# Optimization experiments

Measured on AMD Instinct MI355X. Metric: run time of the kernel, lower is better.

## Reference

```python
import jax, jax.numpy as jnp
import numpy as np

N = 16384          # total points
B = 2              # scans; points[:,0] is batch id
K = 16             # knn neighbors (includes self, dist 0)
CH = [4, 16, 16, 32, 32]
EPS = 1e-5


def setup_inputs() -> dict:
    key = jax.random.key(0)
    ks = jax.random.split(key, 1 + len(CH) - 1)
    feat = jax.random.normal(ks[0], (N, 4), dtype=jnp.float32)
    bidx = jnp.repeat(jnp.arange(B, dtype=jnp.float32), N // B)
    points = jnp.concatenate([bidx[:, None], feat], axis=1)  # [N,5]
    inp = {"points": points}
    for i in range(len(CH) - 1):
        in_c, out_c = CH[i], CH[i + 1]
        inp[f"W{i}"] = jax.random.normal(ks[1 + i], (out_c, 2 * in_c), dtype=jnp.float32) * 0.1
        inp[f"b{i}"] = jnp.zeros((out_c,), dtype=jnp.float32)
        inp[f"g{i}"] = jnp.ones((out_c,), dtype=jnp.float32)
        inp[f"t{i}"] = jnp.zeros((out_c,), dtype=jnp.float32)
    return inp


def _knn(pos, bidx, k):
    # batched brute-force knn: mask cross-batch pairs with +inf
    d2 = jnp.sum(pos * pos, axis=-1)
    dist = d2[:, None] + d2[None, :] - 2.0 * (pos @ pos.T)  # [N,N]
    dist = jnp.where(bidx[:, None] == bidx[None, :], dist, jnp.inf)
    return jax.lax.top_k(-dist, k)[1]  # [N,k] indices of nearest


def _edge_conv(x, idx, W, b, g, t):
    # x: [N,C]; idx: [N,k]
    xi = x[:, None, :]                                   # [N,1,C]
    e = jnp.concatenate(
        [jnp.broadcast_to(xi, idx.shape + (x.shape[-1],)), x[idx] - xi], axis=-1
    )                                                    # [N,k,2C]
    h = jnp.einsum('nke,oe->nko', e, W) + b              # [N,k,out]
    mu = h.mean(axis=(0, 1))
    var = h.var(axis=(0, 1))
    h = (h - mu) * jax.lax.rsqrt(var + EPS) * g + t      # batch-norm (train mode)
    return jnp.max(jax.nn.relu(h), axis=1)               # max over neighbors -> [N,out]


def reference(points, W0, b0, g0, t0, W1, b1, g1, t1, W2, b2, g2, t2, W3, b3, g3, t3):
    bidx = points[:, 0].astype(jnp.int32)
    pos = points[:, 1:4]
    idx = _knn(pos, bidx, K)
    x = points[:, 1:]  # [N,4]
    for W, b, g, t in ((W0, b0, g0, t0), (W1, b1, g1, t1), (W2, b2, g2, t2), (W3, b3, g3, t3)):
        x = _edge_conv(x, idx, W, b, g, t)
    return x  # [N,32] == batch_dict['gcn_feature']
```

## Files before the change

### kernel.cpp

```cpp
#include <hip/hip_runtime.h>
#include <math.h>

typedef unsigned long long u64;

#define N_PTS 16384
#define HALF_N 8192
#define KK 16
#define NK (N_PTS * KK)
#define EPSV 1e-5f
#define FINF 0x7f800000u

#define TGRP 32
#define TGC 64
#define CQB 8
#define CTILE 512
#define CAP 384

#define OFF_IDX   0u
#define OFF_PC    (1u << 20)
#define OFF_MA    (OFF_PC + N_PTS * 16u)
#define OFF_MB    (OFF_MA + N_PTS * 16u * 4u)
#define OFF_MC    (OFF_MB + N_PTS * 16u * 4u)
#define OFF_PART  (OFF_MC + N_PTS * 32u * 4u)
#define OFF_STATS (OFF_PART + 1024u * 64u * 4u)

__global__ __launch_bounds__(256) void prep_kernel(const float* __restrict__ pts,
                                                   float4* __restrict__ pc) {
    int i = blockIdx.x * 256 + threadIdx.x;
    float x = pts[i * 5 + 1], y = pts[i * 5 + 2], z = pts[i * 5 + 3];
    float d2 = __fadd_rn(__fadd_rn(__fmul_rn(x, x), __fmul_rn(y, y)), __fmul_rn(z, z));
    pc[i] = make_float4(x, y, z, d2);
}

__device__ __forceinline__ unsigned fkey(unsigned u) {
    return u ^ ((unsigned)(((int)u) >> 31) | 0x80000000u);
}

__device__ __forceinline__ void cef32(float& a, float& b) {
    float t = fminf(a, b);
    b = fmaxf(a, b);
    a = t;
}

__device__ __forceinline__ void sort8f(float* b) {
    cef32(b[0], b[1]); cef32(b[2], b[3]); cef32(b[4], b[5]); cef32(b[6], b[7]);
    cef32(b[0], b[2]); cef32(b[1], b[3]); cef32(b[4], b[6]); cef32(b[5], b[7]);
    cef32(b[1], b[2]); cef32(b[5], b[6]);
    cef32(b[0], b[4]); cef32(b[1], b[5]); cef32(b[2], b[6]); cef32(b[3], b[7]);
    cef32(b[2], b[4]); cef32(b[3], b[5]);
    cef32(b[1], b[2]); cef32(b[3], b[4]); cef32(b[5], b[6]);
}

__device__ __forceinline__ void sort16f(float b[16]) {
    sort8f(b); sort8f(b + 8);
#pragma unroll
    for (int j = 0; j < 8; ++j) cef32(b[j], b[15 - j]);
#pragma unroll
    for (int h = 0; h < 16; h += 8) {
        cef32(b[h + 0], b[h + 4]); cef32(b[h + 1], b[h + 5]);
        cef32(b[h + 2], b[h + 6]); cef32(b[h + 3], b[h + 7]);
        cef32(b[h + 0], b[h + 2]); cef32(b[h + 1], b[h + 3]);
        cef32(b[h + 4], b[h + 6]); cef32(b[h + 5], b[h + 7]);
        cef32(b[h + 0], b[h + 1]); cef32(b[h + 2], b[h + 3]);
        cef32(b[h + 4], b[h + 5]); cef32(b[h + 6], b[h + 7]);
    }
}

__global__ __launch_bounds__(256, 8) void tau1_kernel(const float4* __restrict__ pc,
                                                      float* __restrict__ gsubT) {
    const int qb = blockIdx.x >> 5;
    const int g  = blockIdx.x & (TGRP - 1);
    const int n  = qb * 256 + threadIdx.x;
    const int base = (n >= HALF_N) ? HALF_N : 0;
    const float4 p = pc[n];

    float m = __uint_as_float(FINF);
    const int c0 = base + g * TGC;
#pragma unroll 8
    for (int t = 0; t < TGC; ++t) {
        const float4 cp = pc[c0 + t];
        float dot = __fadd_rn(__fadd_rn(__fmul_rn(p.x, cp.x), __fmul_rn(p.y, cp.y)),
                              __fmul_rn(p.z, cp.z));
        float dist = __fsub_rn(__fadd_rn(p.w, cp.w), __fmul_rn(2.0f, dot));
        m = fminf(m, dist);
    }
    gsubT[g * N_PTS + n] = m;
}

__global__ __launch_bounds__(256, 4) void tau2_kernel(const float* __restrict__ gsubT,
                                                      float* __restrict__ tauArr) {
    const int n = blockIdx.x * 256 + threadIdx.x;
    float A[16], B[16];
#pragma unroll
    for (int g = 0; g < 16; ++g) A[g] = gsubT[g * N_PTS + n];
#pragma unroll
    for (int g = 0; g < 16; ++g) B[g] = gsubT[(16 + g) * N_PTS + n];
    sort16f(A);
    sort16f(B);
    float tau = __uint_as_float(0xff800000u);
#pragma unroll
    for (int j = 0; j < 16; ++j) tau = fmaxf(tau, fminf(A[j], B[15 - j]));
    tauArr[n] = tau;
}

__global__ __launch_bounds__(512, 8) void collect_kernel(const float4* __restrict__ pc,
                                                         const float* __restrict__ tauArr,
                                                         int* __restrict__ idx) {
    __shared__ float4 tile[CTILE];
    __shared__ u64 lists[CQB][CAP];

    const int tid  = threadIdx.x;
    const int lane = tid & 63;
    const int w    = tid >> 6;
    const int n    = blockIdx.x * CQB + w;
    const int base = (blockIdx.x >= (HALF_N / CQB)) ? HALF_N : 0;
    const float4 p = pc[n];
    const float tauf = tauArr[n];

    u64* list = lists[w];
    int cnt = 0;

    for (int t0 = 0; t0 < HALF_N; t0 += CTILE) {
        __syncthreads();
        tile[tid] = pc[base + t0 + tid];
        __syncthreads();
#pragma unroll
        for (int tt = 0; tt < CTILE; tt += 64) {
            const float4 cp = tile[tt + lane];
            float dot = __fadd_rn(__fadd_rn(__fmul_rn(p.x, cp.x), __fmul_rn(p.y, cp.y)),
                                  __fmul_rn(p.z, cp.z));
            float dist = __fsub_rn(__fadd_rn(p.w, cp.w), __fmul_rn(2.0f, dot));
            const bool acc = !(dist > tauf);
            u64 mask = __ballot(acc);
            if (acc) {
                int slot = cnt + __popcll(mask & ((1ull << lane) - 1ull));
                if (slot < CAP) {
                    const int ci = base + t0 + tt + lane;
                    list[slot] = ((u64)fkey(__float_as_uint(dist)) << 32) | (unsigned)ci;
                }
            }
            cnt += (int)__popcll(mask);
        }
    }

    const int K = min(cnt, CAP);
    for (int e = lane; e < K; e += 64) {
        u64 my = list[e];
        int rank = 0;
        for (int i = 0; i < K; ++i) rank += (list[i] < my) ? 1 : 0;
        if (rank < 16) idx[n * KK + rank] = (int)(my & 0xffffffffULL);
    }
}

template <int IN_C, int OUT_C, int MODE>
__global__ __launch_bounds__(256) void convS_kernel(const float* __restrict__ xin,
                                                    const float* __restrict__ statsPrev,
                                                    const int* __restrict__ idxg,
                                                    const float* __restrict__ W,
                                                    const float* __restrict__ bb,
                                                    float* __restrict__ part,
                                                    float* __restrict__ mout) {
    constexpr int RED = 256 / OUT_C;
    __shared__ float hbuf[OUT_C][257];
    __shared__ float pr1[OUT_C][RED + 1];
    __shared__ float pr2[OUT_C][RED + 1];
    __shared__ float2 sAB[IN_C];

    const int tid = threadIdx.x;
    const int gt = blockIdx.x * 256 + tid;
    const int n = gt >> 4;

    if (MODE == 1) {
        if (tid < IN_C) sAB[tid] = make_float2(statsPrev[tid], statsPrev[32 + tid]);
        __syncthreads();
    }

    float xn[IN_C], dx[IN_C];
    const int j = idxg[gt];
    if (MODE == 0) {
        const float* rn = xin + n * 5 + 1;
        const float* rj = xin + j * 5 + 1;
#pragma unroll
        for (int e = 0; e < IN_C; ++e) xn[e] = rn[e];
#pragma unroll
        for (int e = 0; e < IN_C; ++e) dx[e] = rj[e] - xn[e];
    } else {
        const float4* rn = (const float4*)(xin + n * IN_C);
        const float4* rj = (const float4*)(xin + j * IN_C);
#pragma unroll
        for (int e4 = 0; e4 < IN_C / 4; ++e4) {
            float4 a = rn[e4];
            float4 bq = rj[e4];
            float av[4] = {a.x, a.y, a.z, a.w};
            float bv[4] = {bq.x, bq.y, bq.z, bq.w};
#pragma unroll
            for (int u = 0; u < 4; ++u) {
                float2 ab = sAB[4 * e4 + u];
                float xv = fmaxf(fmaf(av[u], ab.x, ab.y), 0.f);
                float jv = fmaxf(fmaf(bv[u], ab.x, ab.y), 0.f);
                xn[4 * e4 + u] = xv;
                dx[4 * e4 + u] = jv - xv;
            }
        }
    }

    float h[OUT_C];
#pragma unroll
    for (int c = 0; c < OUT_C; ++c) {
        float acc = bb[c];
#pragma unroll
        for (int e = 0; e < IN_C; ++e) acc = fmaf(W[c * 2 * IN_C + e], xn[e], acc);
#pragma unroll
        for (int e = 0; e < IN_C; ++e) acc = fmaf(W[c * 2 * IN_C + IN_C + e], dx[e], acc);
        h[c] = acc;
    }

#pragma unroll
    for (int c = 0; c < OUT_C; ++c) hbuf[c][tid] = h[c];
    __syncthreads();
    {
        const int c2 = tid & (OUT_C - 1);
        const int ch = tid / OUT_C;
        float s1 = 0.f, s2 = 0.f;
#pragma unroll
        for (int i = 0; i < OUT_C; ++i) {
            float hh = hbuf[c2][ch * OUT_C + i];
            s1 += hh; s2 += hh * hh;
        }
        pr1[c2][ch] = s1;
        pr2[c2][ch] = s2;
    }
    __syncthreads();
    if (tid < OUT_C) {
        float t1 = 0.f, t2 = 0.f;
#pragma unroll
        for (int k = 0; k < RED; ++k) { t1 += pr1[tid][k]; t2 += pr2[tid][k]; }
        part[blockIdx.x * 64 + tid]      = t1;
        part[blockIdx.x * 64 + 32 + tid] = t2;
    }

    {
        const int n0 = blockIdx.x * 16;
        constexpr int ITER = OUT_C / 16;
#pragma unroll
        for (int r = 0; r < ITER; ++r) {
            const int c = tid & (OUT_C - 1);
            const int nl = (tid / OUT_C) + r * (256 / OUT_C);
            float m = hbuf[c][nl * 16];
#pragma unroll
            for (int k = 1; k < 16; ++k) m = fmaxf(m, hbuf[c][nl * 16 + k]);
            mout[(n0 + nl) * OUT_C + c] = m;
        }
    }
}

__global__ __launch_bounds__(256) void finalize_kernel(const float* __restrict__ part,
                                                       const float* __restrict__ g,
                                                       const float* __restrict__ t,
                                                       float* __restrict__ statsL) {
    __shared__ float s1[128], s2[128];
    const int c = blockIdx.x;
    const int tid = threadIdx.x;

    if (tid < 128) {
        float a = 0.f;
#pragma unroll
        for (int i = 0; i < 8; ++i) a += part[(tid * 8 + i) * 64 + c];
        s1[tid] = a;
    } else {
        const int t2 = tid - 128;
        float a = 0.f;
#pragma unroll
        for (int i = 0; i < 8; ++i) a += part[(t2 * 8 + i) * 64 + 32 + c];
        s2[t2] = a;
    }
    __syncthreads();
    for (int st = 64; st >= 1; st >>= 1) {
        if (tid < st) s1[tid] += s1[tid + st];
        else if (tid >= 128 && tid < 128 + st) s2[tid - 128] += s2[tid - 128 + st];
        __syncthreads();
    }
    if (tid == 0) {
        const float inv = 1.0f / (float)NK;
        float mu  = s1[0] * inv;
        float var = s2[0] * inv - mu * mu;
        float rs  = 1.0f / sqrtf(var + EPSV);
        float A   = rs * g[c];
        statsL[c]      = A;
        statsL[32 + c] = t[c] - mu * A;
    }
}

__global__ __launch_bounds__(256) void apply_kernel(const float* __restrict__ m,
                                                    const float* __restrict__ st,
                                                    float* __restrict__ out) {
    const int i = blockIdx.x * 256 + threadIdx.x;
    float4 mv = ((const float4*)m)[i];
    const int c0 = (i * 4) & 31;
    float4 Av = *(const float4*)(st + c0);
    float4 Bv = *(const float4*)(st + 32 + c0);
    float4 o;
    o.x = fmaxf(fmaf(mv.x, Av.x, Bv.x), 0.f);
    o.y = fmaxf(fmaf(mv.y, Av.y, Bv.y), 0.f);
    o.z = fmaxf(fmaf(mv.z, Av.z, Bv.z), 0.f);
    o.w = fmaxf(fmaf(mv.w, Av.w, Bv.w), 0.f);
    ((float4*)out)[i] = o;
}

extern "C" void kernel_launch(void* const* d_in, const int* in_sizes, int n_in,
                              void* d_out, int out_size, void* d_ws, size_t ws_size,
                              hipStream_t stream) {
    const float* pts = (const float*)d_in[0];
    const float* Wl[4], *bl[4], *gl[4], *tl[4];
    for (int l = 0; l < 4; ++l) {
        Wl[l] = (const float*)d_in[1 + 4 * l + 0];
        bl[l] = (const float*)d_in[1 + 4 * l + 1];
        gl[l] = (const float*)d_in[1 + 4 * l + 2];
        tl[l] = (const float*)d_in[1 + 4 * l + 3];
    }
    char* ws = (char*)d_ws;
    int*    idx    = (int*)(ws + OFF_IDX);
    float4* pc     = (float4*)(ws + OFF_PC);
    float*  gsubT  = (float*)(ws + OFF_MA);
    float*  m0     = (float*)(ws + OFF_MA);
    float*  m1     = (float*)(ws + OFF_MB);
    float*  m2     = (float*)(ws + OFF_MC);
    float*  m3     = (float*)(ws + OFF_MA);
    float*  part   = (float*)(ws + OFF_PART);
    float*  tauArr = (float*)(ws + OFF_PART);
    float*  stats  = (float*)(ws + OFF_STATS);
    float*  out    = (float*)d_out;

    prep_kernel<<<N_PTS / 256, 256, 0, stream>>>(pts, pc);
    tau1_kernel<<<(N_PTS / 256) * TGRP, 256, 0, stream>>>(pc, gsubT);
    tau2_kernel<<<N_PTS / 256, 256, 0, stream>>>(gsubT, tauArr);
    collect_kernel<<<N_PTS / CQB, 512, 0, stream>>>(pc, tauArr, idx);

    const int GA = NK / 256;

    convS_kernel<4, 16, 0><<<GA, 256, 0, stream>>>(pts, nullptr, idx, Wl[0], bl[0], part, m0);
    finalize_kernel<<<16, 256, 0, stream>>>(part, gl[0], tl[0], stats + 0);

    convS_kernel<16, 16, 1><<<GA, 256, 0, stream>>>(m0, stats + 0, idx, Wl[1], bl[1], part, m1);
    finalize_kernel<<<16, 256, 0, stream>>>(part, gl[1], tl[1], stats + 64);

    convS_kernel<16, 32, 1><<<GA, 256, 0, stream>>>(m1, stats + 64, idx, Wl[2], bl[2], part, m2);
    finalize_kernel<<<32, 256, 0, stream>>>(part, gl[2], tl[2], stats + 128);

    convS_kernel<32, 32, 1><<<GA, 256, 0, stream>>>(m2, stats + 128, idx, Wl[3], bl[3], part, m3);
    finalize_kernel<<<32, 256, 0, stream>>>(part, gl[3], tl[3], stats + 192);

    apply_kernel<<<(N_PTS * 32 / 4) / 256, 256, 0, stream>>>(m3, stats + 192, out);
}
```

Baseline: 192.7 us.

## Process four queries per wavefront in kNN collect, drop LDS candidate tile

```diff
diff --git a/kernel.cpp b/kernel.cpp
--- a/kernel.cpp
+++ b/kernel.cpp
@@ -12,9 +12,9 @@
 
 #define TGRP 32
 #define TGC 64
-#define CQB 8
-#define CTILE 512
-#define CAP 384
+#define QW 4
+#define QBLK 16
+#define CAP 288
 
 #define OFF_IDX   0u
 #define OFF_PC    (1u << 20)
@@ -103,53 +103,77 @@
     tauArr[n] = tau;
 }
 
-__global__ __launch_bounds__(512, 8) void collect_kernel(const float4* __restrict__ pc,
+__global__ __launch_bounds__(256, 4) void collect_kernel(const float4* __restrict__ pc,
                                                          const float* __restrict__ tauArr,
                                                          int* __restrict__ idx) {
-    __shared__ float4 tile[CTILE];
-    __shared__ u64 lists[CQB][CAP];
+    __shared__ u64 lists[QBLK][CAP];
 
     const int tid  = threadIdx.x;
     const int lane = tid & 63;
     const int w    = tid >> 6;
-    const int n    = blockIdx.x * CQB + w;
-    const int base = (blockIdx.x >= (HALF_N / CQB)) ? HALF_N : 0;
-    const float4 p = pc[n];
-    const float tauf = tauArr[n];
-
-    u64* list = lists[w];
-    int cnt = 0;
-
-    for (int t0 = 0; t0 < HALF_N; t0 += CTILE) {
-        __syncthreads();
-        tile[tid] = pc[base + t0 + tid];
-        __syncthreads();
-#pragma unroll
-        for (int tt = 0; tt < CTILE; tt += 64) {
-            const float4 cp = tile[tt + lane];
-            float dot = __fadd_rn(__fadd_rn(__fmul_rn(p.x, cp.x), __fmul_rn(p.y, cp.y)),
-                                  __fmul_rn(p.z, cp.z));
-            float dist = __fsub_rn(__fadd_rn(p.w, cp.w), __fmul_rn(2.0f, dot));
-            const bool acc = !(dist > tauf);
-            u64 mask = __ballot(acc);
-            if (acc) {
-                int slot = cnt + __popcll(mask & ((1ull << lane) - 1ull));
-                if (slot < CAP) {
-                    const int ci = base + t0 + tt + lane;
-                    list[slot] = ((u64)fkey(__float_as_uint(dist)) << 32) | (unsigned)ci;
-                }
-            }
-            cnt += (int)__popcll(mask);
+    const int nb   = blockIdx.x * QBLK + w * QW;
+    const int base = (blockIdx.x >= (HALF_N / QBLK)) ? HALF_N : 0;
+
+    const float4 q0 = pc[nb + 0], q1 = pc[nb + 1], q2 = pc[nb + 2], q3 = pc[nb + 3];
+    const float tau0 = tauArr[nb + 0], tau1 = tauArr[nb + 1];
+    const float tau2 = tauArr[nb + 2], tau3 = tauArr[nb + 3];
+
+    u64* l0 = lists[w * QW + 0];
+    u64* l1 = lists[w * QW + 1];
+    u64* l2 = lists[w * QW + 2];
+    u64* l3 = lists[w * QW + 3];
+    int c0 = 0, c1 = 0, c2 = 0, c3 = 0;
+
+    const u64 lt = (1ull << lane) - 1ull;
+
+    for (int t0 = 0; t0 < HALF_N; t0 += 64) {
+        const int ci = base + t0 + lane;
+        const float4 cp = pc[ci];
+
+#define DIST(Q) (__fsub_rn(__fadd_rn(Q.w, cp.w), __fmul_rn(2.0f,                      \
+            __fadd_rn(__fadd_rn(__fmul_rn(Q.x, cp.x), __fmul_rn(Q.y, cp.y)),          \
+                      __fmul_rn(Q.z, cp.z)))))
+        const float d0 = DIST(q0);
+        const float d1 = DIST(q1);
+        const float d2 = DIST(q2);
+        const float d3 = DIST(q3);
+#undef DIST
+
+#define APPEND(D, TAU, LST, CNT)                                                      \
+        {                                                                             \
+            const bool acc = !((D) > (TAU));                                          \
+            const u64 mask = __ballot(acc);                                           \
+            if (mask) {                                                               \
+                if (acc) {                                                            \
+                    int slot = (CNT) + (int)__popcll(mask & lt);                      \
+                    if (slot < CAP)                                                   \
+                        (LST)[slot] = ((u64)fkey(__float_as_uint(D)) << 32) | (unsigned)ci; \
+                }                                                                     \
+                (CNT) += (int)__popcll(mask);                                         \
+            }                                                                         \
         }
-    }
-
-    const int K = min(cnt, CAP);
-    for (int e = lane; e < K; e += 64) {
-        u64 my = list[e];
-        int rank = 0;
-        for (int i = 0; i < K; ++i) rank += (list[i] < my) ? 1 : 0;
-        if (rank < 16) idx[n * KK + rank] = (int)(my & 0xffffffffULL);
-    }
+        APPEND(d0, tau0, l0, c0)
+        APPEND(d1, tau1, l1, c1)
+        APPEND(d2, tau2, l2, c2)
+        APPEND(d3, tau3, l3, c3)
+#undef APPEND
+    }
+
+#define SELECT(LST, CNT, QI)                                                          \
+    {                                                                                 \
+        const int K = min((CNT), CAP);                                                \
+        for (int e = lane; e < K; e += 64) {                                          \
+            u64 my = (LST)[e];                                                        \
+            int rank = 0;                                                             \
+            for (int i = 0; i < K; ++i) rank += ((LST)[i] < my) ? 1 : 0;              \
+            if (rank < 16) idx[(nb + (QI)) * KK + rank] = (int)(my & 0xffffffffULL);  \
+        }                                                                             \
+    }
+    SELECT(l0, c0, 0)
+    SELECT(l1, c1, 1)
+    SELECT(l2, c2, 2)
+    SELECT(l3, c3, 3)
+#undef SELECT
 }
 
 template <int IN_C, int OUT_C, int MODE>
@@ -334,7 +358,7 @@
     prep_kernel<<<N_PTS / 256, 256, 0, stream>>>(pts, pc);
     tau1_kernel<<<(N_PTS / 256) * TGRP, 256, 0, stream>>>(pc, gsubT);
     tau2_kernel<<<N_PTS / 256, 256, 0, stream>>>(gsubT, tauArr);
-    collect_kernel<<<N_PTS / CQB, 512, 0, stream>>>(pc, tauArr, idx);
+    collect_kernel<<<N_PTS / QBLK, 256, 0, stream>>>(pc, tauArr, idx);
 
     const int GA = NK / 256;
 
```

After: 195.8 us. About the same (+1.6%).
